# Kernel tuning notes

Measured on AMD Instinct MI355X. Metric: run time of the kernel, lower is better.

The kernel has to match this reference:

```python
import jax, jax.numpy as jnp
import numpy as np

B, T, F, L = 512, 512, 128, 512  # batch, seq_len, n_features, latent_dim


def setup_inputs() -> dict:
    key = jax.random.key(0)
    ks = jax.random.split(key, 8)
    s = 1.0 / np.sqrt(L)  # torch default init scale for GRUCell (hidden_size=L)
    sd = 1.0 / np.sqrt(L)  # torch Linear(L, F) init scale
    return {
        "x": jax.random.normal(ks[0], (B, T, F), jnp.float32),
        "h_0": jax.random.normal(ks[1], (1, B, L), jnp.float32),
        "W_ih": jax.random.uniform(ks[2], (3 * L, F), jnp.float32, -s, s),
        "W_hh": jax.random.uniform(ks[3], (3 * L, L), jnp.float32, -s, s),
        "b_ih": jax.random.uniform(ks[4], (3 * L,), jnp.float32, -s, s),
        "b_hh": jax.random.uniform(ks[5], (3 * L,), jnp.float32, -s, s),
        "Wd": jax.random.uniform(ks[6], (F, L), jnp.float32, -sd, sd),
        "bd": jax.random.uniform(ks[7], (F,), jnp.float32, -sd, sd),
        "seq_len": T,
    }


def reference(x, h_0, W_ih, W_hh, b_ih, b_hh, Wd, bd, seq_len):
    # epsilon=0.0 default: teacher forcing never fires, so x_t = dense(h_t).
    h = jnp.squeeze(h_0, axis=0)          # [B, L]
    xt = h @ Wd.T + bd                    # [B, F]  (initial dense(h_0))

    def step(carry, _):
        h, xt = carry
        gi = xt @ W_ih.T + b_ih           # [B, 3L]
        gh = h @ W_hh.T + b_hh            # [B, 3L]
        i_r, i_z, i_n = jnp.split(gi, 3, axis=-1)
        h_r, h_z, h_n = jnp.split(gh, 3, axis=-1)
        r = jax.nn.sigmoid(i_r + h_r)
        z = jax.nn.sigmoid(i_z + h_z)
        n = jnp.tanh(i_n + r * h_n)
        h_new = (1.0 - z) * n + z * h     # [B, L]
        x_new = h_new @ Wd.T + bd         # [B, F] == dense(h_t) == output[:, t]
        return (h_new, x_new), x_new

    _, ys = jax.lax.scan(step, (h, xt), None, length=seq_len)  # ys: [T, B, F]
    return jnp.transpose(ys, (1, 0, 2))   # [B, T, F]
```

## Files before the change

kernel.cpp:

```cpp
#include <hip/hip_runtime.h>
#include <stdint.h>

typedef _Float16 f16;
typedef _Float16 half8 __attribute__((ext_vector_type(8)));
typedef _Float16 half4 __attribute__((ext_vector_type(4)));
typedef float float4v __attribute__((ext_vector_type(4)));
typedef float float2v __attribute__((ext_vector_type(2)));
typedef unsigned int u32;

#define MFMA16(A, B, C) __builtin_amdgcn_mfma_f32_16x16x32_f16((A), (B), (C), 0, 0, 0)

static constexpr int Bsz = 512, Tsz = 512, Fsz = 128, Lsz = 512;
static constexpr int NPACK = 2176;
static constexpr float LO_S = 2048.0f, LO_R = 1.0f / 2048.0f;

static constexpr size_t WSZ_FRAG  = (size_t)(NPACK / 16) * 16 * 64 * 8 * 2;
static constexpr size_t OFF_WHI   = 0;
static constexpr size_t OFF_WLO   = OFF_WHI + WSZ_FRAG;
static constexpr size_t OFF_BIAS  = OFF_WLO + WSZ_FRAG;
static constexpr size_t OFF_HHI   = OFF_BIAS + 16384;
static constexpr size_t OFF_HLO   = OFF_HHI + (size_t)2 * Bsz * Lsz * 2;
static constexpr size_t OFF_FLAGS = OFF_HLO + (size_t)2 * Bsz * Lsz * 2;

static constexpr int EXS = 37;
static constexpr int LDS_HI = 0;
static constexpr int LDS_LO = 32768;
static constexpr int LDS_EX = 65536;
static constexpr int LDS_YP = LDS_EX + 16 * 32 * EXS * 4;
static constexpr int LDS_TOT = LDS_YP + 4 * 32 * 17 * 4;

__device__ __host__ __forceinline__ int swz(int c, int r) {
  return (((c >> 3) ^ (r & 7)) << 3) | (c & 7);
}

__device__ __forceinline__ void async16(const void* g, void* l) {
  __builtin_amdgcn_global_load_lds((const __attribute__((address_space(1))) u32*)g,
                                   (__attribute__((address_space(3))) u32*)l, 16, 0, 16);
}

__device__ __forceinline__ float sigm(float x) { return 1.0f / (1.0f + __expf(-x)); }
__device__ __forceinline__ float tanh_(float x) { return 1.0f - 2.0f / (__expf(2.0f * x) + 1.0f); }

__global__ void k_pack(const float* __restrict__ Wih, const float* __restrict__ Whh,
                       const float* __restrict__ Wd, f16* __restrict__ whiF,
                       f16* __restrict__ wloF) {
  const int c = blockIdx.y;
  const int l = blockIdx.x * 256 + threadIdx.x;
  float v;
  if (c < 1536) {
    const float* wih = Wih + c * 128;
    float acc = 0.f;
#pragma unroll 8
    for (int f = 0; f < 128; ++f) acc = fmaf(Wd[f * 512 + l], wih[f], acc);
    v = acc;
    if (c < 1024) v += Whh[c * 512 + l];
  } else if (c < 2048) {
    v = Whh[(c - 512) * 512 + l];
  } else {
    v = Wd[(c - 2048) * 512 + l];
  }
  f16 hi = (f16)v;
  f16 lo = (f16)((v - (float)hi) * LO_S);
  const int chunk = c >> 4, ks = l >> 5, q = (l >> 3) & 3, j = l & 7, n = c & 15;
  const size_t idx = (((size_t)(chunk * 16 + ks)) * 64 + q * 16 + n) * 8 + j;
  whiF[idx] = hi;
  wloF[idx] = lo;
}

__global__ void k_init(const float* __restrict__ h0, const float* __restrict__ Wih,
                       const float* __restrict__ bih, const float* __restrict__ bhh,
                       const float* __restrict__ bd, f16* __restrict__ hhi,
                       f16* __restrict__ hlo, float* __restrict__ biasP,
                       int* __restrict__ flags) {
  const int t = blockIdx.x * 256 + threadIdx.x;
  if (t < Bsz * Lsz) {
    const int row = t >> 9, col = t & 511;
    float v = h0[t];
    f16 hi = (f16)v;
    f16 lo = (f16)((v - (float)hi) * LO_S);
    const int cp = swz(col, row);
    hhi[row * 512 + cp] = hi;
    hlo[row * 512 + cp] = lo;
  }
  if (t < NPACK) {
    float v;
    if (t < 1536) {
      float a = bih[t];
      for (int f = 0; f < 128; ++f) a = fmaf(Wih[t * 128 + f], bd[f], a);
      if (t < 1024) a += bhh[t];
      v = a;
    } else if (t < 2048) {
      v = bhh[t - 512];
    } else {
      v = bd[t - 2048];
    }
    biasP[t] = v;
  }
  if (t < 8192) flags[t] = 0;
}

__global__ __launch_bounds__(256, 1) void k_main(
    const float* __restrict__ h0, const f16* __restrict__ whiF,
    const f16* __restrict__ wloF, const float* __restrict__ biasP,
    f16* __restrict__ hhi, f16* __restrict__ hlo, int* __restrict__ flags,
    float* __restrict__ out) {
  extern __shared__ char dsm[];
  f16* sHi = (f16*)(dsm + LDS_HI);
  f16* sLo = (f16*)(dsm + LDS_LO);
  float* ex = (float*)(dsm + LDS_EX);
  float* yp = (float*)(dsm + LDS_YP);

  const int bid = blockIdx.x;
  const int g = bid & 15;
  const int m = bid >> 4;
  const int tid = threadIdx.x;
  const int v = tid >> 6, lane = tid & 63, q = lane >> 4, n = lane & 15;

  const half8* whiV = (const half8*)whiF;
  const half8* wloV = (const half8*)wloF;
  half8 w_hi[4][2][4], w_lo[4][2][4];
#pragma unroll
  for (int t = 0; t < 4; ++t)
#pragma unroll
    for (int nt = 0; nt < 2; ++nt)
#pragma unroll
      for (int ks = 0; ks < 4; ++ks) {
        const int idx = ((t * 32 + m * 2 + nt) * 16 + v * 4 + ks) * 64 + lane;
        w_hi[t][nt][ks] = whiV[idx];
        w_lo[t][nt][ks] = wloV[idx];
      }
  half8 w_y[4];
  if (m < 8) {
#pragma unroll
    for (int ks = 0; ks < 4; ++ks) w_y[ks] = whiV[((128 + m) * 16 + v * 4 + ks) * 64 + lane];
  }

  const int rl = tid >> 3, c0 = (tid & 7) * 4;
  float bias[4][4];
#pragma unroll
  for (int t = 0; t < 4; ++t)
#pragma unroll
    for (int cc = 0; cc < 4; ++cc) bias[t][cc] = biasP[t * 512 + m * 32 + c0 + cc];
  float hreg[4];
#pragma unroll
  for (int cc = 0; cc < 4; ++cc)
    hreg[cc] = h0[(size_t)(32 * g + rl) * 512 + m * 32 + c0 + cc];
  const int c2 = (tid & 7) * 2;
  float by[2] = {0.f, 0.f};
  if (m < 8) {
    by[0] = biasP[2048 + m * 16 + c2];
    by[1] = biasP[2048 + m * 16 + c2 + 1];
  }

  int* gcnt = flags + g * 64;
  const size_t rowbaseB = (size_t)(32 * g) * 1024;

  for (int s = 1; s <= 513; ++s) {
    {
      const char* srcHi = (const char*)hhi + (size_t)((s - 1) & 1) * 524288 + rowbaseB;
      const char* srcLo = (const char*)hlo + (size_t)((s - 1) & 1) * 524288 + rowbaseB;
      const int off = v * 8192 + lane * 16;
#pragma unroll
      for (int i = 0; i < 8; ++i) {
        async16(srcHi + off + i * 1024, dsm + LDS_HI + off + i * 1024);
        async16(srcLo + off + i * 1024, dsm + LDS_LO + off + i * 1024);
      }
    }
    __syncthreads();

#pragma unroll
    for (int p = 0; p < 2; ++p) {
      float4v a_hh[2][2][2], a_ll[2][2][2];
#pragma unroll
      for (int ti = 0; ti < 2; ++ti)
#pragma unroll
        for (int nt = 0; nt < 2; ++nt)
#pragma unroll
          for (int mt = 0; mt < 2; ++mt) {
            a_hh[ti][nt][mt] = (float4v){0,0,0,0};
            a_ll[ti][nt][mt] = (float4v){0,0,0,0};
          }
#pragma unroll
      for (int ks = 0; ks < 4; ++ks) {
        half8 ah[2], al[2];
#pragma unroll
        for (int mt = 0; mt < 2; ++mt) {
          const int offE = (mt * 16 + n) * 512 + ((((v * 4 + ks) * 4 + q) ^ (n & 7)) * 8);
          ah[mt] = *(const half8*)(sHi + offE);
          al[mt] = *(const half8*)(sLo + offE);
        }
#pragma unroll
        for (int ti = 0; ti < 2; ++ti) {
          const int t = p * 2 + ti;
#pragma unroll
          for (int nt = 0; nt < 2; ++nt)
#pragma unroll
            for (int mt = 0; mt < 2; ++mt) {
              a_hh[ti][nt][mt] = MFMA16(ah[mt], w_hi[t][nt][ks], a_hh[ti][nt][mt]);
              a_ll[ti][nt][mt] = MFMA16(al[mt], w_hi[t][nt][ks], a_ll[ti][nt][mt]);
              a_ll[ti][nt][mt] = MFMA16(ah[mt], w_lo[t][nt][ks], a_ll[ti][nt][mt]);
            }
        }
      }
#pragma unroll
      for (int ti = 0; ti < 2; ++ti) {
        const int t = p * 2 + ti;
#pragma unroll
        for (int nt = 0; nt < 2; ++nt)
#pragma unroll
          for (int mt = 0; mt < 2; ++mt) {
            const int base = ((t * 4 + v) * 32 + nt * 16 + n) * EXS + mt * 16 + q * 4;
            const float4v vv = a_hh[ti][nt][mt] + a_ll[ti][nt][mt] * LO_R;
            *(float2v*)(ex + base) = (float2v){vv[0], vv[1]};
            *(float2v*)(ex + base + 2) = (float2v){vv[2], vv[3]};
          }
      }
    }
    __syncthreads();

    float pre[4][4];
#pragma unroll
    for (int t = 0; t < 4; ++t)
#pragma unroll
      for (int cc = 0; cc < 4; ++cc) {
        float acc = bias[t][cc];
#pragma unroll
        for (int w = 0; w < 4; ++w) acc += ex[((t * 4 + w) * 32 + c0 + cc) * EXS + rl];
        pre[t][cc] = acc;
      }
    const int rg = 32 * g + rl;
    half4 hiv, lov;
#pragma unroll
    for (int cc = 0; cc < 4; ++cc) {
      const float r = sigm(pre[0][cc]);
      const float z = sigm(pre[1][cc]);
      const float nn = tanh_(fmaf(r, pre[3][cc], pre[2][cc]));
      const float hn = fmaf(z, hreg[cc] - nn, nn);
      hreg[cc] = hn;
      const f16 hi = (f16)hn;
      hiv[cc] = hi;
      lov[cc] = (f16)((hn - (float)hi) * LO_S);
    }
    {
      const int colp = swz(m * 32 + c0, rg);
      const size_t o = (size_t)(s & 1) * 262144 + (size_t)rg * 512 + colp;
      __hip_atomic_store((uint64_t*)(hhi + o), __builtin_bit_cast(uint64_t, hiv),
                         __ATOMIC_RELAXED, __HIP_MEMORY_SCOPE_AGENT);
      __hip_atomic_store((uint64_t*)(hlo + o), __builtin_bit_cast(uint64_t, lov),
                         __ATOMIC_RELAXED, __HIP_MEMORY_SCOPE_AGENT);
    }
    asm volatile("s_waitcnt vmcnt(0)" ::: "memory");
    __syncthreads();
    if (tid == 0)
      __hip_atomic_fetch_add(gcnt, 1, __ATOMIC_RELAXED, __HIP_MEMORY_SCOPE_AGENT);

    if (m < 8) {
      float4v yac[2] = {(float4v){0,0,0,0}, (float4v){0,0,0,0}};
#pragma unroll
      for (int ks = 0; ks < 4; ++ks) {
#pragma unroll
        for (int mt = 0; mt < 2; ++mt) {
          const int offE = (mt * 16 + n) * 512 + ((((v * 4 + ks) * 4 + q) ^ (n & 7)) * 8);
          const half8 ah = *(const half8*)(sHi + offE);
          yac[mt] = MFMA16(ah, w_y[ks], yac[mt]);
        }
      }
#pragma unroll
      for (int mt = 0; mt < 2; ++mt)
#pragma unroll
        for (int e = 0; e < 4; ++e)
          yp[(v * 32 + mt * 16 + q * 4 + e) * 17 + n] = yac[mt][e];
    }
    __syncthreads();

    if (m < 8 && s >= 2) {
#pragma unroll
      for (int cc = 0; cc < 2; ++cc) {
        float yv = by[cc];
#pragma unroll
        for (int w = 0; w < 4; ++w) yv += yp[(w * 32 + rl) * 17 + c2 + cc];
        __builtin_nontemporal_store(
            yv, out + (size_t)rg * (Tsz * Fsz) + (size_t)(s - 2) * Fsz + m * 16 + c2 + cc);
      }
    }

    if (s < 513) {
      if (tid == 0) {
        while (__hip_atomic_load(gcnt, __ATOMIC_RELAXED, __HIP_MEMORY_SCOPE_AGENT) <
               16 * s)
          __builtin_amdgcn_s_sleep(1);
      }
      __syncthreads();
    }
  }
}

extern "C" void kernel_launch(void* const* d_in, const int* in_sizes, int n_in,
                              void* d_out, int out_size, void* d_ws, size_t ws_size,
                              hipStream_t stream) {
  (void)in_sizes; (void)n_in; (void)out_size; (void)ws_size;
  const float* h0  = (const float*)d_in[1];
  const float* Wih = (const float*)d_in[2];
  const float* Whh = (const float*)d_in[3];
  const float* bih = (const float*)d_in[4];
  const float* bhh = (const float*)d_in[5];
  const float* Wd  = (const float*)d_in[6];
  const float* bd  = (const float*)d_in[7];
  float* out = (float*)d_out;
  char* ws = (char*)d_ws;

  f16* whiF    = (f16*)(ws + OFF_WHI);
  f16* wloF    = (f16*)(ws + OFF_WLO);
  float* biasP = (float*)(ws + OFF_BIAS);
  f16* hhi     = (f16*)(ws + OFF_HHI);
  f16* hlo     = (f16*)(ws + OFF_HLO);
  int* flags   = (int*)(ws + OFF_FLAGS);

  hipFuncSetAttribute((const void*)k_main, hipFuncAttributeMaxDynamicSharedMemorySize,
                      LDS_TOT);
  k_pack<<<dim3(2, NPACK), 256, 0, stream>>>(Wih, Whh, Wd, whiF, wloF);
  k_init<<<1024, 256, 0, stream>>>(h0, Wih, bih, bhh, bd, hhi, hlo, biasP, flags);
  k_main<<<256, 256, LDS_TOT, stream>>>(h0, whiF, wloF, biasP, hhi, hlo, flags, out);
}
```

Measured before the change: 4.687 ms.

## Replace group barrier with per-producer flags and fragment-ordered interleaved h buffer

Packs the hi and lo halves of the hidden state into one buffer laid out in MFMA fragment order, with hi and lo interleaved per record. Each block now publishes a per-block step flag, and each wave waits only on the four producer blocks whose columns it loads before issuing that chunk's async loads. This replaces the group-wide atomic counter and the spin at the end of the step. The aim is to shorten the critical path of the per-step cross-block synchronisation and let loads start as soon as individual producers finish. The risk is more flag polling traffic and subtle ordering or race issues, since the block-wide barrier before the LDS reads is removed and each wave reads only its own staged chunk.

```diff
diff --git a/kernel.cpp b/kernel.cpp
--- a/kernel.cpp
+++ b/kernel.cpp
@@ -18,20 +18,15 @@
 static constexpr size_t OFF_WHI   = 0;
 static constexpr size_t OFF_WLO   = OFF_WHI + WSZ_FRAG;
 static constexpr size_t OFF_BIAS  = OFF_WLO + WSZ_FRAG;
-static constexpr size_t OFF_HHI   = OFF_BIAS + 16384;
-static constexpr size_t OFF_HLO   = OFF_HHI + (size_t)2 * Bsz * Lsz * 2;
-static constexpr size_t OFF_FLAGS = OFF_HLO + (size_t)2 * Bsz * Lsz * 2;
-
+static constexpr size_t OFF_HX    = OFF_BIAS + 16384;
+static constexpr size_t OFF_FLAGS = OFF_HX + (size_t)2 * 1024 * 1024;
+
+
+static constexpr int LDS_H  = 0;
 static constexpr int EXS = 37;
-static constexpr int LDS_HI = 0;
-static constexpr int LDS_LO = 32768;
 static constexpr int LDS_EX = 65536;
 static constexpr int LDS_YP = LDS_EX + 16 * 32 * EXS * 4;
 static constexpr int LDS_TOT = LDS_YP + 4 * 32 * 17 * 4;
-
-__device__ __host__ __forceinline__ int swz(int c, int r) {
-  return (((c >> 3) ^ (r & 7)) << 3) | (c & 7);
-}
 
 __device__ __forceinline__ void async16(const void* g, void* l) {
   __builtin_amdgcn_global_load_lds((const __attribute__((address_space(1))) u32*)g,
@@ -69,18 +64,20 @@
 
 __global__ void k_init(const float* __restrict__ h0, const float* __restrict__ Wih,
                        const float* __restrict__ bih, const float* __restrict__ bhh,
-                       const float* __restrict__ bd, f16* __restrict__ hhi,
-                       f16* __restrict__ hlo, float* __restrict__ biasP,
-                       int* __restrict__ flags) {
+                       const float* __restrict__ bd, f16* __restrict__ hx,
+                       float* __restrict__ biasP, int* __restrict__ flags) {
   const int t = blockIdx.x * 256 + threadIdx.x;
   if (t < Bsz * Lsz) {
     const int row = t >> 9, col = t & 511;
     float v = h0[t];
     f16 hi = (f16)v;
     f16 lo = (f16)((v - (float)hi) * LO_S);
-    const int cp = swz(col, row);
-    hhi[row * 512 + cp] = hi;
-    hlo[row * 512 + cp] = lo;
+    const int g = row >> 5, rl = row & 31, mt = rl >> 4, n = rl & 15;
+    const int mm = col >> 5, cs = col & 31, qq = (cs >> 3) ^ (n & 3), j = cs & 7;
+    const size_t b = (size_t)g * 65536 + (size_t)mm * 4096 + mt * 2048 + n * 128 + qq * 32;
+    char* p = (char*)hx + b;
+    *(f16*)(p + j * 2) = hi;
+    *(f16*)(p + 16 + j * 2) = lo;
   }
   if (t < NPACK) {
     float v;
@@ -102,11 +99,8 @@
 __global__ __launch_bounds__(256, 1) void k_main(
     const float* __restrict__ h0, const f16* __restrict__ whiF,
     const f16* __restrict__ wloF, const float* __restrict__ biasP,
-    f16* __restrict__ hhi, f16* __restrict__ hlo, int* __restrict__ flags,
-    float* __restrict__ out) {
+    f16* __restrict__ hx, int* __restrict__ flags, float* __restrict__ out) {
   extern __shared__ char dsm[];
-  f16* sHi = (f16*)(dsm + LDS_HI);
-  f16* sLo = (f16*)(dsm + LDS_LO);
   float* ex = (float*)(dsm + LDS_EX);
   float* yp = (float*)(dsm + LDS_YP);
 
@@ -152,21 +146,31 @@
     by[1] = biasP[2048 + m * 16 + c2 + 1];
   }
 
-  int* gcnt = flags + g * 64;
-  const size_t rowbaseB = (size_t)(32 * g) * 1024;
+  const int mtP = rl >> 4, nP = rl & 15;
+  const size_t recO = (size_t)m * 4096 + mtP * 2048 + nP * 128 +
+                      (((c0 >> 3) ^ (nP & 3)) * 32) + (((c0 >> 2) & 1) * 8);
+  const int fragB0 = LDS_H + v * 16384 + n * 128 + ((q ^ (n & 3)) * 32);
+
+  int* myflag = flags + (g * 16 + m) * 16;
+  const size_t grpB = (size_t)g * 65536;
 
   for (int s = 1; s <= 513; ++s) {
     {
-      const char* srcHi = (const char*)hhi + (size_t)((s - 1) & 1) * 524288 + rowbaseB;
-      const char* srcLo = (const char*)hlo + (size_t)((s - 1) & 1) * 524288 + rowbaseB;
-      const int off = v * 8192 + lane * 16;
-#pragma unroll
-      for (int i = 0; i < 8; ++i) {
-        async16(srcHi + off + i * 1024, dsm + LDS_HI + off + i * 1024);
-        async16(srcLo + off + i * 1024, dsm + LDS_LO + off + i * 1024);
-      }
-    }
-    __syncthreads();
+      const size_t bufB = (size_t)((s - 1) & 1) * 1048576 + grpB;
+#pragma unroll
+      for (int j = 0; j < 4; ++j) {
+        const int* fa = flags + (g * 16 + (4 * v + j)) * 16;
+        while (__hip_atomic_load(fa, __ATOMIC_RELAXED, __HIP_MEMORY_SCOPE_AGENT) < s - 1)
+          __builtin_amdgcn_s_sleep(1);
+        __builtin_amdgcn_sched_barrier(0);
+        const char* src = (const char*)hx + bufB + (size_t)(4 * v + j) * 4096 + lane * 16;
+        char* dst = dsm + LDS_H + v * 16384 + j * 4096 + lane * 16;
+#pragma unroll
+        for (int i = 0; i < 4; ++i) async16(src + i * 1024, dst + i * 1024);
+      }
+    }
+    asm volatile("s_waitcnt vmcnt(0)" ::: "memory");
+    __builtin_amdgcn_sched_barrier(0);
 
 #pragma unroll
     for (int p = 0; p < 2; ++p) {
@@ -185,9 +189,9 @@
         half8 ah[2], al[2];
 #pragma unroll
         for (int mt = 0; mt < 2; ++mt) {
-          const int offE = (mt * 16 + n) * 512 + ((((v * 4 + ks) * 4 + q) ^ (n & 7)) * 8);
-          ah[mt] = *(const half8*)(sHi + offE);
-          al[mt] = *(const half8*)(sLo + offE);
+          const char* fp = dsm + fragB0 + ks * 4096 + mt * 2048;
+          ah[mt] = *(const half8*)fp;
+          al[mt] = *(const half8*)(fp + 16);
         }
 #pragma unroll
         for (int ti = 0; ti < 2; ++ti) {
@@ -242,17 +246,16 @@
       lov[cc] = (f16)((hn - (float)hi) * LO_S);
     }
     {
-      const int colp = swz(m * 32 + c0, rg);
-      const size_t o = (size_t)(s & 1) * 262144 + (size_t)rg * 512 + colp;
-      __hip_atomic_store((uint64_t*)(hhi + o), __builtin_bit_cast(uint64_t, hiv),
+      const size_t ob = (size_t)(s & 1) * 1048576 + grpB + recO;
+      __hip_atomic_store((uint64_t*)((char*)hx + ob), __builtin_bit_cast(uint64_t, hiv),
                          __ATOMIC_RELAXED, __HIP_MEMORY_SCOPE_AGENT);
-      __hip_atomic_store((uint64_t*)(hlo + o), __builtin_bit_cast(uint64_t, lov),
+      __hip_atomic_store((uint64_t*)((char*)hx + ob + 16), __builtin_bit_cast(uint64_t, lov),
                          __ATOMIC_RELAXED, __HIP_MEMORY_SCOPE_AGENT);
     }
     asm volatile("s_waitcnt vmcnt(0)" ::: "memory");
     __syncthreads();
     if (tid == 0)
-      __hip_atomic_fetch_add(gcnt, 1, __ATOMIC_RELAXED, __HIP_MEMORY_SCOPE_AGENT);
+      __hip_atomic_store(myflag, s, __ATOMIC_RELAXED, __HIP_MEMORY_SCOPE_AGENT);
 
     if (m < 8) {
       float4v yac[2] = {(float4v){0,0,0,0}, (float4v){0,0,0,0}};
@@ -260,8 +263,7 @@
       for (int ks = 0; ks < 4; ++ks) {
 #pragma unroll
         for (int mt = 0; mt < 2; ++mt) {
-          const int offE = (mt * 16 + n) * 512 + ((((v * 4 + ks) * 4 + q) ^ (n & 7)) * 8);
-          const half8 ah = *(const half8*)(sHi + offE);
+          const half8 ah = *(const half8*)(dsm + fragB0 + ks * 4096 + mt * 2048);
           yac[mt] = MFMA16(ah, w_y[ks], yac[mt]);
         }
       }
@@ -282,15 +284,6 @@
         __builtin_nontemporal_store(
             yv, out + (size_t)rg * (Tsz * Fsz) + (size_t)(s - 2) * Fsz + m * 16 + c2 + cc);
       }
-    }
-
-    if (s < 513) {
-      if (tid == 0) {
-        while (__hip_atomic_load(gcnt, __ATOMIC_RELAXED, __HIP_MEMORY_SCOPE_AGENT) <
-               16 * s)
-          __builtin_amdgcn_s_sleep(1);
-      }
-      __syncthreads();
     }
   }
 }
@@ -312,13 +305,12 @@
   f16* whiF    = (f16*)(ws + OFF_WHI);
   f16* wloF    = (f16*)(ws + OFF_WLO);
   float* biasP = (float*)(ws + OFF_BIAS);
-  f16* hhi     = (f16*)(ws + OFF_HHI);
-  f16* hlo     = (f16*)(ws + OFF_HLO);
+  f16* hx      = (f16*)(ws + OFF_HX);
   int* flags   = (int*)(ws + OFF_FLAGS);
 
   hipFuncSetAttribute((const void*)k_main, hipFuncAttributeMaxDynamicSharedMemorySize,
                       LDS_TOT);
   k_pack<<<dim3(2, NPACK), 256, 0, stream>>>(Wih, Whh, Wd, whiF, wloF);
-  k_init<<<1024, 256, 0, stream>>>(h0, Wih, bih, bhh, bd, hhi, hlo, biasP, flags);
-  k_main<<<256, 256, LDS_TOT, stream>>>(h0, whiF, wloF, biasP, hhi, hlo, flags, out);
-}
+  k_init<<<1024, 256, 0, stream>>>(h0, Wih, bih, bhh, bd, hx, biasP, flags);
+  k_main<<<256, 256, LDS_TOT, stream>>>(h0, whiF, wloF, biasP, hx, flags, out);
+}
```

Result: slower. 4.806 ms (+2.6%).
